# Performance work log

Measured on AMD Instinct MI355X. Metric: run time of the kernel, lower is better.

The kernel has to match this reference:

```python
import jax, jax.numpy as jnp
import numpy as np

SEQ_LEN, PRED_LEN = 512, 96
D_MODEL, D_STATE, D_FF = 512, 16, 512
DT_RANK = 32  # ceil(d_model / 16)
E_LAYERS = 2
B, N = 32, 256


def _layernorm(x, g, b, eps=1e-5):
    mu = jnp.mean(x, -1, keepdims=True)
    var = jnp.mean((x - mu) ** 2, -1, keepdims=True)
    return (x - mu) * jax.lax.rsqrt(var + eps) * g + b


def _mamba(x, win, convw, convb, wx, wdt, bdt, alog, dparam, wout):
    # x: [B, T, D] with T = n_variates + 6 (inverted tokens)
    Bb, T, D = x.shape
    xz = x @ win.T                      # [B, T, 2D] (expand=1 -> d_inner = D)
    xr, z = xz[..., :D], xz[..., D:]
    # causal depthwise conv, d_conv=2: y[t] = w0*x[t-1] + w1*x[t] + b
    x_prev = jnp.pad(xr, ((0, 0), (1, 0), (0, 0)))[:, :T]
    xc = jax.nn.silu(x_prev * convw[:, 0] + xr * convw[:, 1] + convb)
    dbl = xc @ wx.T                     # [B, T, dt_rank + 2*d_state]
    dt = jax.nn.softplus(dbl[..., :DT_RANK] @ wdt.T + bdt)     # [B, T, D]
    Bm = dbl[..., DT_RANK:DT_RANK + D_STATE]                    # [B, T, S]
    Cm = dbl[..., DT_RANK + D_STATE:]                           # [B, T, S]
    A = -jnp.exp(alog)                                          # [D, S]
    dA = jnp.exp(dt[..., None] * A)                             # [B, T, D, S]
    dBx = dt[..., None] * Bm[:, :, None, :] * xc[..., None]     # [B, T, D, S]

    def step(h, inp):
        a_t, bx_t = inp
        h = a_t * h + bx_t
        return h, h

    h0 = jnp.zeros((Bb, D, D_STATE), x.dtype)
    _, hs = jax.lax.scan(step, h0, (jnp.swapaxes(dA, 0, 1), jnp.swapaxes(dBx, 0, 1)))
    y = jnp.einsum('tbds,bts->btd', hs, Cm) + dparam * xc
    y = y * jax.nn.silu(z)
    return y @ wout.T


def _forward(x_enc, x_mark_enc, emb_w, emb_b, m_win, m_convw, m_convb, m_wx, m_wdt,
             m_bdt, m_alog, m_dparam, m_wout, ln1_g, ln1_b, ff1_w, ff1_b, ff2_w,
             ff2_b, ln2_g, ln2_b, lnf_g, lnf_b, proj_w, proj_b):
    n_var = x_enc.shape[2]
    # instance norm over time (use_norm=True)
    means = jnp.mean(x_enc, 1, keepdims=True)
    xn = x_enc - means
    stdev = jnp.sqrt(jnp.var(xn, axis=1, keepdims=True) + 1e-5)
    xn = xn / stdev
    # inverted embedding: tokens = variates (+ time-feature channels), proj seq_len -> d_model
    tok = jnp.concatenate([jnp.swapaxes(xn, 1, 2), jnp.swapaxes(x_mark_enc, 1, 2)], axis=1)
    h = tok @ emb_w.T + emb_b           # [B, n_var+6, d_model]
    for l in range(E_LAYERS):
        f = _mamba(h, m_win[l, 0], m_convw[l, 0], m_convb[l, 0], m_wx[l, 0],
                   m_wdt[l, 0], m_bdt[l, 0], m_alog[l, 0], m_dparam[l, 0], m_wout[l, 0])
        r = jnp.flip(_mamba(jnp.flip(h, 1), m_win[l, 1], m_convw[l, 1], m_convb[l, 1],
                            m_wx[l, 1], m_wdt[l, 1], m_bdt[l, 1], m_alog[l, 1],
                            m_dparam[l, 1], m_wout[l, 1]), 1)
        h = _layernorm(h + f + r, ln1_g[l], ln1_b[l])
        y = jax.nn.relu(h @ ff1_w[l].T + ff1_b[l]) @ ff2_w[l].T + ff2_b[l]
        h = _layernorm(h + y, ln2_g[l], ln2_b[l])
    h = _layernorm(h, lnf_g, lnf_b)
    dec = jnp.swapaxes(h @ proj_w.T + proj_b, 1, 2)[:, :, :n_var]  # [B, pred_len, N]
    dec = dec * stdev[:, 0, :][:, None, :] + means[:, 0, :][:, None, :]
    return dec


def setup_inputs() -> dict:
    key = jax.random.key(0)
    ks = iter(jax.random.split(key, 64))

    def rn(shape, scale=0.02):
        return jax.random.normal(next(ks), shape, dtype=jnp.float32) * scale

    D, S, R, L = D_MODEL, D_STATE, DT_RANK, E_LAYERS
    return dict(
        x_enc=jax.random.normal(next(ks), (B, SEQ_LEN, N), dtype=jnp.float32),
        x_mark_enc=jax.random.uniform(next(ks), (B, SEQ_LEN, 6), dtype=jnp.float32,
                                      minval=-1.0, maxval=1.0),
        emb_w=rn((D, SEQ_LEN)), emb_b=jnp.zeros((D,), jnp.float32),
        m_win=rn((L, 2, 2 * D, D)),
        m_convw=rn((L, 2, D, 2), 0.5),
        m_convb=jnp.zeros((L, 2, D), jnp.float32),
        m_wx=rn((L, 2, R + 2 * S, D)),
        m_wdt=rn((L, 2, D, R)),
        m_bdt=jnp.full((L, 2, D), -4.6, jnp.float32),  # softplus ~= 0.01
        m_alog=jnp.broadcast_to(jnp.log(jnp.arange(1, S + 1, dtype=jnp.float32)), (L, 2, D, S)) * jnp.ones((L, 2, D, S), jnp.float32),
        m_dparam=jnp.ones((L, 2, D), jnp.float32),
        m_wout=rn((L, 2, D, D)),
        ln1_g=jnp.ones((L, D), jnp.float32), ln1_b=jnp.zeros((L, D), jnp.float32),
        ff1_w=rn((L, D_FF, D)), ff1_b=jnp.zeros((L, D_FF), jnp.float32),
        ff2_w=rn((L, D, D_FF)), ff2_b=jnp.zeros((L, D), jnp.float32),
        ln2_g=jnp.ones((L, D), jnp.float32), ln2_b=jnp.zeros((L, D), jnp.float32),
        lnf_g=jnp.ones((D,), jnp.float32), lnf_b=jnp.zeros((D,), jnp.float32),
        proj_w=rn((PRED_LEN, D)), proj_b=jnp.zeros((PRED_LEN,), jnp.float32),
    )


def reference(x_enc, x_mark_enc, emb_w, emb_b, m_win, m_convw, m_convb, m_wx, m_wdt,
              m_bdt, m_alog, m_dparam, m_wout, ln1_g, ln1_b, ff1_w, ff1_b, ff2_w,
              ff2_b, ln2_g, ln2_b, lnf_g, lnf_b, proj_w, proj_b):
    return _forward(x_enc, x_mark_enc, emb_w, emb_b, m_win, m_convw, m_convb, m_wx,
                    m_wdt, m_bdt, m_alog, m_dparam, m_wout, ln1_g, ln1_b, ff1_w,
                    ff1_b, ff2_w, ff2_b, ln2_g, ln2_b, lnf_g, lnf_b, proj_w, proj_b)
```

## Files before the change

kernel.cpp:

```cpp
#include <hip/hip_runtime.h>
#include <hip/hip_bf16.h>
#include <math.h>
#include <stddef.h>

#define BB 32
#define TT 262
#define DD 512
#define SS 16
#define RR 32
#define SEQ 512
#define NV 256
#define PRED 96
#define MROWS (BB*TT)
#define NCHK 8
#define CSZ 33

typedef __attribute__((ext_vector_type(4))) float f32x4;
typedef __attribute__((ext_vector_type(8))) short s16x8;

__device__ inline ushort f2bu(float x) {
    __hip_bfloat16 h = __float2bfloat16(x);
    ushort u; __builtin_memcpy(&u, &h, 2); return u;
}
__device__ inline float bu2f(ushort u) {
    __hip_bfloat16 h; __builtin_memcpy(&h, &u, 2);
    return __bfloat162float(h);
}

__device__ inline void gload_lds16(const void* g, void* l) {
    __builtin_amdgcn_global_load_lds(
        (const __attribute__((address_space(1))) void*)g,
        (__attribute__((address_space(3))) void*)l, 16, 0, 0);
}

__global__ __launch_bounds__(256)
void packall(const float* __restrict__ s0, ushort* __restrict__ d0,
             const float* __restrict__ s1, ushort* __restrict__ d1,
             const float* __restrict__ s2, ushort* __restrict__ d2,
             const float* __restrict__ s3, ushort* __restrict__ d3,
             const float* __restrict__ s4, ushort* __restrict__ d4,
             const float* __restrict__ s5, ushort* __restrict__ d5)
{
    int idx = blockIdx.x * 256 + threadIdx.x;
    const float* s; ushort* dst; int o;
    if      (idx < 262144)  { s = s0; dst = d0; o = idx; }
    else if (idx < 2359296) { s = s1; dst = d1; o = idx - 262144; }
    else if (idx < 3407872) { s = s2; dst = d2; o = idx - 2359296; }
    else if (idx < 3932160) { s = s3; dst = d3; o = idx - 3407872; }
    else if (idx < 4456448) { s = s4; dst = d4; o = idx - 3932160; }
    else if (idx < 4505600) { s = s5; dst = d5; o = idx - 4456448; }
    else return;
    dst[o] = f2bu(s[o]);
}

__global__ __launch_bounds__(256)
void mkcomb(const float* __restrict__ wx, const float* __restrict__ wdt,
            ushort* __restrict__ comb)
{
    int n  = blockIdx.x;
    int li = blockIdx.y;
    const float* wxl = wx + (size_t)li*64*512;
    ushort* outb = comb + ((size_t)li*544 + n)*512;
    if (n < 512) {
        __shared__ float wr[32];
        if (threadIdx.x < 32)
            wr[threadIdx.x] = wdt[(size_t)li*512*32 + (size_t)n*32 + threadIdx.x];
        __syncthreads();
        for (int kk = threadIdx.x; kk < 512; kk += 256) {
            float acc = 0.f;
            #pragma unroll
            for (int r = 0; r < 32; ++r)
                acc = fmaf(wr[r], wxl[r*512 + kk], acc);
            outb[kk] = f2bu(acc);
        }
    } else {
        int s = n - 512;
        for (int kk = threadIdx.x; kk < 512; kk += 256)
            outb[kk] = f2bu(wxl[(32+s)*512 + kk]);
    }
}

__global__ __launch_bounds__(256)
void stats_kernel(const float* __restrict__ x_enc,
                  float* __restrict__ mean, float* __restrict__ stdv)
{
    int b  = blockIdx.x >> 4;
    int n0 = (blockIdx.x & 15) << 4;
    int nl = threadIdx.x & 15;
    int tg = threadIdx.x >> 4;
    int n = n0 + nl;
    const float* base = x_enc + (size_t)b*SEQ*NV + n;
    float s0 = 0.f, s1 = 0.f, q0 = 0.f, q1 = 0.f;
    #pragma unroll 8
    for (int i = 0; i < 16; ++i) {
        int t = tg + i*32;
        float v0 = base[(size_t)t*NV];
        float v1 = base[(size_t)(t+16)*NV];
        s0 += v0; q0 = fmaf(v0, v0, q0);
        s1 += v1; q1 = fmaf(v1, v1, q1);
    }
    float s = s0 + s1, q = q0 + q1;
    __shared__ float ls[16][17], lq[16][17];
    ls[tg][nl] = s; lq[tg][nl] = q;
    __syncthreads();
    if (tg < 8) { ls[tg][nl] += ls[tg+8][nl]; lq[tg][nl] += lq[tg+8][nl]; }
    __syncthreads();
    if (tg < 4) { ls[tg][nl] += ls[tg+4][nl]; lq[tg][nl] += lq[tg+4][nl]; }
    __syncthreads();
    if (tg < 2) { ls[tg][nl] += ls[tg+2][nl]; lq[tg][nl] += lq[tg+2][nl]; }
    __syncthreads();
    if (tg == 0) {
        s = ls[0][nl] + ls[1][nl];
        q = lq[0][nl] + lq[1][nl];
        float mu  = s * (1.f/SEQ);
        float var = q * (1.f/SEQ) - mu*mu;
        mean[b*NV + n] = mu;
        stdv[b*NV + n] = sqrtf(var + 1e-5f);
    }
}

__global__ __launch_bounds__(256)
void tok_kernel(const float* __restrict__ x_enc, const float* __restrict__ x_mark,
                const float* __restrict__ mean, const float* __restrict__ stdv,
                ushort* __restrict__ tokb)
{
    int b  = blockIdx.x / 40;
    int r  = blockIdx.x % 40;
    int tt = r / 5;
    int vt = r % 5;
    int t0 = tt << 6, v0 = vt << 6;
    __shared__ float tile[64][65];
    int lv = threadIdx.x & 63;
    for (int i = threadIdx.x >> 6; i < 64; i += 4) {
        int t = t0 + i, v = v0 + lv;
        float val = 0.f;
        if (v < NV) {
            val = (x_enc[((size_t)b*SEQ + t)*NV + v] - mean[b*NV + v]) / stdv[b*NV + v];
        } else if (v < TT) {
            val = x_mark[((size_t)b*SEQ + t)*6 + (v - NV)];
        }
        tile[i][lv] = val;
    }
    __syncthreads();
    for (int i = threadIdx.x >> 6; i < 64; i += 4) {
        int v = v0 + i;
        if (v < TT) {
            size_t row = (size_t)b*TT + v;
            tokb[row*512 + t0 + lv] = f2bu(tile[lv][i]);
        }
    }
}

template<int HAS_BIAS, int RELU, int WF32, int W3, int SCANEP>
__global__ __launch_bounds__(256)
void gemm3(const ushort* __restrict__ A3, int lda3,
           const ushort* __restrict__ W3p, int ldw3,
           const float* __restrict__ bias,
           float* __restrict__ C, int ldc,
           ushort* __restrict__ C3, int N_out,
           float* __restrict__ bcbuf,
           size_t aOff, size_t wOff, size_t biasOff, size_t cOff, size_t bcOff,
           int M, int Nn, int K3)
{
    const int dir = blockIdx.y;
    A3  += (size_t)dir * aOff;
    W3p += (size_t)dir * wOff;
    if (HAS_BIAS || SCANEP) bias += (size_t)dir * biasOff;
    if (WF32) C += (size_t)dir * cOff;
    if (W3 || SCANEP) C3 += (size_t)dir * cOff;
    if (SCANEP) bcbuf += (size_t)dir * bcOff;

    __shared__ ushort lds[2][192*64];
    const int tid  = threadIdx.x;
    const int lane = tid & 63;
    const int wid  = tid >> 6;
    const int wr = wid >> 1, wc = wid & 1;

    int nwg = gridDim.x;
    int q8 = nwg >> 3, r8 = nwg & 7;
    int xcd = blockIdx.x & 7;
    int idx = blockIdx.x >> 3;
    int swz = (xcd < r8 ? xcd*(q8+1) : r8*(q8+1) + (xcd-r8)*q8) + idx;
    int ntile = (Nn + 63) >> 6;
    const int m0 = (swz / ntile) * 128;
    const int n0 = (swz % ntile) * 64;

    const int l8 = lane >> 3;
    const int sl = lane & 7;
    const int ssl = sl ^ l8;

    int arow[4], wrow[2];
    #pragma unroll
    for (int qq = 0; qq < 4; ++qq) {
        int r = (wid*4 + qq)*8 + l8;
        int ar = m0 + r; if (ar > M-1) ar = M-1;
        arow[qq] = ar;
    }
    #pragma unroll
    for (int qq = 0; qq < 2; ++qq) {
        int r = (wid*2 + qq)*8 + l8;
        int wrr = n0 + r; if (wrr > Nn-1) wrr = Nn-1;
        wrow[qq] = wrr;
    }

    f32x4 acc[4][2];
    #pragma unroll
    for (int i = 0; i < 4; ++i)
        #pragma unroll
        for (int j = 0; j < 2; ++j) acc[i][j] = (f32x4){0.f,0.f,0.f,0.f};

    const int nk = K3 >> 6;
    const int rl = lane & 15;
    const int kq = lane >> 4;

    auto stage = [&](int buf_, int kt_) {
        #pragma unroll
        for (int qq = 0; qq < 4; ++qq) {
            int c = wid*4 + qq;
            gload_lds16(A3 + (size_t)arow[qq]*lda3 + kt_*64 + ssl*8,
                        (void*)&lds[buf_][c*512]);
        }
        #pragma unroll
        for (int qq = 0; qq < 2; ++qq) {
            int c = wid*2 + qq;
            gload_lds16(W3p + (size_t)wrow[qq]*ldw3 + kt_*64 + ssl*8,
                        (void*)&lds[buf_][8192 + c*512]);
        }
    };

    stage(0, 0);
    __syncthreads();

    for (int kt = 0; kt < nk; ++kt) {
        int cur = kt & 1;
        if (kt + 1 < nk) stage(cur ^ 1, kt + 1);
        #pragma unroll
        for (int kk = 0; kk < 2; ++kk) {
            s16x8 av[4], wv[2];
            #pragma unroll
            for (int mi = 0; mi < 4; ++mi) {
                int row = wr*64 + mi*16 + rl;
                int ck = (kk*4 + kq) ^ (row & 7);
                av[mi] = *(const s16x8*)&lds[cur][row*64 + (ck<<3)];
            }
            #pragma unroll
            for (int ni = 0; ni < 2; ++ni) {
                int row = wc*32 + ni*16 + rl;
                int ck = (kk*4 + kq) ^ (row & 7);
                wv[ni] = *(const s16x8*)&lds[cur][8192 + row*64 + (ck<<3)];
            }
            #pragma unroll
            for (int mi = 0; mi < 4; ++mi)
                #pragma unroll
                for (int ni = 0; ni < 2; ++ni)
                    acc[mi][ni] = __builtin_amdgcn_mfma_f32_16x16x32_bf16(
                        av[mi], wv[ni], acc[mi][ni], 0, 0, 0);
        }
        __syncthreads();
    }

    #pragma unroll
    for (int ni = 0; ni < 2; ++ni) {
        int n = n0 + wc*32 + ni*16 + rl;
        if (n >= Nn) continue;
        float bv = (HAS_BIAS && !SCANEP) ? bias[n] : 0.f;
        #pragma unroll
        for (int mi = 0; mi < 4; ++mi) {
            #pragma unroll
            for (int j = 0; j < 4; ++j) {
                int m = m0 + wr*64 + mi*16 + kq*4 + j;
                if (m >= M) continue;
                float v = acc[mi][ni][j];
                if (SCANEP) {
                    if (n < 512) {
                        v += bias[n];
                        v = fmaxf(v, 0.f) + log1pf(__expf(-fabsf(v)));
                        C3[(size_t)m*ldc + n] = f2bu(v);
                    } else {
                        bcbuf[(size_t)m*N_out + (n - 512)] = v;
                    }
                } else {
                    if (HAS_BIAS) v += bv;
                    if (RELU) v = fmaxf(v, 0.f);
                    if (WF32) C[(size_t)m*ldc + n] = v;
                    if (W3)   C3[(size_t)m*N_out + n] = f2bu(v);
                }
            }
        }
    }
}

__global__ __launch_bounds__(256)
void conv2(ushort* __restrict__ xzb, const float* __restrict__ cwB,
           const float* __restrict__ cbB, float* __restrict__ xc,
           ushort* __restrict__ xcb)
{
    int gid = blockIdx.x * 256 + threadIdx.x;
    int d = gid & 511;
    int r = gid >> 9;
    int dir = (r >= MROWS) ? 1 : 0;
    int bt = r - dir*MROWS;
    int t = bt % TT;
    const float* cw = cwB + dir*DD*2;
    const float* cb = cbB + dir*DD;
    size_t base = (size_t)bt*2048 + (size_t)dir*1024;
    float cur = bu2f(xzb[base + d]);
    int tn = dir ? t + 1 : t - 1;
    float prev = 0.f;
    if (tn >= 0 && tn < TT)
        prev = bu2f(xzb[base + (dir ? 2048 : -2048) + d]);
    float v = prev*cw[d*2] + cur*cw[d*2+1] + cb[d];
    float sv = v / (1.f + __expf(-v));
    size_t o = (size_t)bt*1024 + dir*512 + d;
    xc[o] = sv;
    xcb[o] = f2bu(sv);
    float z = bu2f(xzb[base + 512 + d]);
    xzb[base + 512 + d] = f2bu(z / (1.f + __expf(-z)));
}

__global__ __launch_bounds__(64)
void scan_p1(const ushort* __restrict__ sp_g, const float* __restrict__ xc_g,
             const float* __restrict__ bc_g, const float* __restrict__ alog,
             float* __restrict__ hs, float* __restrict__ ps)
{
    int dir = blockIdx.z;
    int rev = dir;
    sp_g += dir*512; xc_g += dir*512; bc_g += dir*32;
    alog += (size_t)dir*DD*SS;
    size_t doff = (size_t)dir*(NCHK-1)*65536*4;
    hs += doff; ps += doff;

    int sblk = blockIdx.x;
    int c    = blockIdx.y;
    int b  = sblk >> 3;
    int d  = ((sblk & 7) << 6) + threadIdx.x;

    float Ac[16];
    #pragma unroll
    for (int j = 0; j < 16; ++j)
        Ac[j] = -__expf(alog[d*SS + j]);

    float h[16], pp[16];
    #pragma unroll
    for (int j = 0; j < 16; ++j) { h[j] = 0.f; pp[j] = 1.f; }

    size_t bbase = (size_t)b*TT;
    int t0 = c*CSZ;
    for (int i = 0; i < CSZ; ++i) {
        int t = t0 + i;
        size_t p = bbase + (rev ? TT-1-t : t);
        float spv = bu2f(sp_g[p*1024 + d]);
        float xcv = xc_g[p*1024 + d];
        const float* bc = bc_g + p*64;
        float dtxc = spv*xcv;
        f32x4 Bq[4];
        #pragma unroll
        for (int q = 0; q < 4; ++q) Bq[q] = ((const f32x4*)bc)[q];
        #pragma unroll
        for (int j = 0; j < 16; ++j) {
            float e = __expf(spv*Ac[j]);
            h[j] = fmaf(e, h[j], dtxc*Bq[j>>2][j&3]);
            pp[j] *= e;
        }
    }
    size_t o = (((size_t)c*256 + sblk)*64 + threadIdx.x)*4;
    #pragma unroll
    for (int q = 0; q < 4; ++q) {
        ((f32x4*)hs)[o + q] = (f32x4){h[q*4+0], h[q*4+1], h[q*4+2], h[q*4+3]};
        ((f32x4*)ps)[o + q] = (f32x4){pp[q*4+0], pp[q*4+1], pp[q*4+2], pp[q*4+3]};
    }
}

__global__ __launch_bounds__(256)
void scan_comb(const float* __restrict__ hs, const float* __restrict__ ps,
               float* __restrict__ hin)
{
    int dir = blockIdx.y;
    size_t doff = (size_t)dir*(NCHK-1)*65536;
    size_t gid = (size_t)blockIdx.x*256 + threadIdx.x;
    float4 h = {0.f,0.f,0.f,0.f};
    for (int c = 0; c < NCHK-1; ++c) {
        size_t o = doff + (size_t)c*65536 + gid;
        float4 hl = ((const float4*)hs)[o];
        float4 pv = ((const float4*)ps)[o];
        h.x = fmaf(pv.x, h.x, hl.x);
        h.y = fmaf(pv.y, h.y, hl.y);
        h.z = fmaf(pv.z, h.z, hl.z);
        h.w = fmaf(pv.w, h.w, hl.w);
        ((float4*)hin)[o] = h;
    }
}

__global__ __launch_bounds__(64)
void scan_p2(const ushort* __restrict__ sp_g, const float* __restrict__ xc_g,
             const ushort* __restrict__ xz_u, const float* __restrict__ bc_g,
             const float* __restrict__ alog, const float* __restrict__ dparam,
             const float* __restrict__ hin, ushort* __restrict__ yb)
{
    int dir = blockIdx.z;
    int rev = dir;
    sp_g += dir*512; xc_g += dir*512; bc_g += dir*32; xz_u += dir*1024;
    alog += (size_t)dir*DD*SS; dparam += (size_t)dir*DD;
    hin += (size_t)dir*(NCHK-1)*65536*4;
    yb  += (size_t)dir*(size_t)MROWS*512;

    int sblk = blockIdx.x;
    int c    = blockIdx.y;
    int b  = sblk >> 3;
    int d  = ((sblk & 7) << 6) + threadIdx.x;

    float Ac[16];
    #pragma unroll
    for (int j = 0; j < 16; ++j)
        Ac[j] = -__expf(alog[d*SS + j]);
    float dp = dparam[d];

    float h[16];
    #pragma unroll
    for (int j = 0; j < 16; ++j) h[j] = 0.f;
    if (c > 0) {
        size_t o = (((size_t)(c-1)*256 + sblk)*64 + threadIdx.x)*4;
        #pragma unroll
        for (int q = 0; q < 4; ++q) {
            f32x4 hv = ((const f32x4*)hin)[o + q];
            h[q*4+0]=hv[0]; h[q*4+1]=hv[1]; h[q*4+2]=hv[2]; h[q*4+3]=hv[3];
        }
    }

    size_t bbase = (size_t)b*TT;
    int t0 = c*CSZ;
    for (int i = 0; i < CSZ; ++i) {
        int t = t0 + i;
        int tc = t < TT ? t : TT-1;
        size_t p = bbase + (rev ? TT-1-tc : tc);
        float spv = bu2f(sp_g[p*1024 + d]);
        float xcv = xc_g[p*1024 + d];
        float zsv = bu2f(xz_u[p*2048 + 512 + d]);
        const float* bc = bc_g + p*64;
        float dtxc = spv*xcv;
        f32x4 Bq[4], Cq[4];
        #pragma unroll
        for (int q = 0; q < 4; ++q) {
            Bq[q] = ((const f32x4*)bc)[q];
            Cq[q] = ((const f32x4*)(bc + 16))[q];
        }
        #pragma unroll
        for (int j = 0; j < 16; ++j) {
            float e = __expf(spv*Ac[j]);
            h[j] = fmaf(e, h[j], dtxc*Bq[j>>2][j&3]);
        }
        float p0 = 0.f, p1 = 0.f, p2 = 0.f, p3 = 0.f;
        #pragma unroll
        for (int q = 0; q < 4; ++q) {
            p0 = fmaf(h[q*4+0], Cq[q][0], p0);
            p1 = fmaf(h[q*4+1], Cq[q][1], p1);
            p2 = fmaf(h[q*4+2], Cq[q][2], p2);
            p3 = fmaf(h[q*4+3], Cq[q][3], p3);
        }
        float dot = (p0 + p1) + (p2 + p3);
        if (t < TT) {
            int tg = rev ? TT-1-t : t;
            float yv = (dot + dp*xcv) * zsv;
            yb[(bbase + tg)*512 + d] = f2bu(yv);
        }
    }
}

__global__ __launch_bounds__(64)
void ln_kernel(float* __restrict__ dst, const float* __restrict__ a,
               const float* __restrict__ b, const float* __restrict__ c,
               const float* __restrict__ g, const float* __restrict__ beta,
               ushort* __restrict__ outb)
{
    int row = blockIdx.x;
    int lane = threadIdx.x;
    size_t base = (size_t)row * DD;
    float x[8];
    #pragma unroll
    for (int j = 0; j < 2; ++j) {
        int e4 = j*64 + lane;
        float4 v = *(const float4*)(a + base + (size_t)e4*4);
        if (b) { float4 t = *(const float4*)(b + base + (size_t)e4*4); v.x+=t.x; v.y+=t.y; v.z+=t.z; v.w+=t.w; }
        if (c) { float4 t = *(const float4*)(c + base + (size_t)e4*4); v.x+=t.x; v.y+=t.y; v.z+=t.z; v.w+=t.w; }
        x[j*4+0]=v.x; x[j*4+1]=v.y; x[j*4+2]=v.z; x[j*4+3]=v.w;
    }
    float s = 0.f;
    #pragma unroll
    for (int i = 0; i < 8; ++i) s += x[i];
    #pragma unroll
    for (int m = 1; m < 64; m <<= 1) s += __shfl_xor(s, m);
    float mu = s * (1.f/DD);
    float vs = 0.f;
    #pragma unroll
    for (int i = 0; i < 8; ++i) { float dd = x[i]-mu; vs += dd*dd; }
    #pragma unroll
    for (int m = 1; m < 64; m <<= 1) vs += __shfl_xor(vs, m);
    float r = rsqrtf(vs*(1.f/DD) + 1e-5f);
    #pragma unroll
    for (int j = 0; j < 2; ++j) {
        int e4 = j*64 + lane;
        float4 gv = *(const float4*)(g    + (size_t)e4*4);
        float4 bv = *(const float4*)(beta + (size_t)e4*4);
        float4 o;
        o.x = (x[j*4+0]-mu)*r*gv.x + bv.x;
        o.y = (x[j*4+1]-mu)*r*gv.y + bv.y;
        o.z = (x[j*4+2]-mu)*r*gv.z + bv.z;
        o.w = (x[j*4+3]-mu)*r*gv.w + bv.w;
        *(float4*)(dst + base + (size_t)e4*4) = o;
        if (outb) {
            ushort* ob = outb + (size_t)row*512;
            ob[e4*4+0] = f2bu(o.x);
            ob[e4*4+1] = f2bu(o.y);
            ob[e4*4+2] = f2bu(o.z);
            ob[e4*4+3] = f2bu(o.w);
        }
    }
}

__global__ __launch_bounds__(256)
void proj_fin(const float* __restrict__ projtmp, const float* __restrict__ mean,
              const float* __restrict__ stdv, float* __restrict__ out)
{
    int b  = blockIdx.x >> 2;
    int n0 = (blockIdx.x & 3) << 6;
    __shared__ float tile[64][97];
    for (int i = threadIdx.x; i < 64*96; i += 256) {
        int rj = i / 96, cp = i % 96;
        tile[rj][cp] = projtmp[((size_t)b*TT + n0 + rj)*96 + cp];
    }
    __syncthreads();
    int nl = threadIdx.x & 63;
    int pg = threadIdx.x >> 6;
    int n = n0 + nl;
    float sd = stdv[b*NV + n];
    float mu = mean[b*NV + n];
    #pragma unroll
    for (int i = 0; i < 24; ++i) {
        int p = pg*24 + i;
        out[((size_t)b*PRED + p)*NV + n] = tile[nl][p]*sd + mu;
    }
}

extern "C" void kernel_launch(void* const* d_in, const int* in_sizes, int n_in,
                              void* d_out, int out_size, void* d_ws, size_t ws_size,
                              hipStream_t stream)
{
    (void)in_sizes; (void)n_in; (void)out_size; (void)ws_size;
    const float* x_enc   = (const float*)d_in[0];
    const float* x_mark  = (const float*)d_in[1];
    const float* emb_w   = (const float*)d_in[2];
    const float* emb_b   = (const float*)d_in[3];
    const float* m_win   = (const float*)d_in[4];
    const float* m_convw = (const float*)d_in[5];
    const float* m_convb = (const float*)d_in[6];
    const float* m_wx    = (const float*)d_in[7];
    const float* m_wdt   = (const float*)d_in[8];
    const float* m_bdt   = (const float*)d_in[9];
    const float* m_alog  = (const float*)d_in[10];
    const float* m_dpar  = (const float*)d_in[11];
    const float* m_wout  = (const float*)d_in[12];
    const float* ln1_g   = (const float*)d_in[13];
    const float* ln1_b   = (const float*)d_in[14];
    const float* ff1_w   = (const float*)d_in[15];
    const float* ff1_b   = (const float*)d_in[16];
    const float* ff2_w   = (const float*)d_in[17];
    const float* ff2_b   = (const float*)d_in[18];
    const float* ln2_g   = (const float*)d_in[19];
    const float* ln2_b   = (const float*)d_in[20];
    const float* lnf_g   = (const float*)d_in[21];
    const float* lnf_b   = (const float*)d_in[22];
    const float* proj_w  = (const float*)d_in[23];
    const float* proj_b  = (const float*)d_in[24];
    float* out = (float*)d_out;

    float* ws = (float*)d_ws;
    const size_t NBT = (size_t)MROWS;
    size_t off = 0;
    float* mean = ws + off; off += 8192;
    float* stdv = ws + off; off += 8192;
    ushort* w_emb  = (ushort*)(ws + off); off += 131072;
    ushort* w_win  = (ushort*)(ws + off); off += 1048576;
    ushort* w_wout = (ushort*)(ws + off); off += 524288;
    ushort* w_ff1  = (ushort*)(ws + off); off += 262144;
    ushort* w_ff2  = (ushort*)(ws + off); off += 262144;
    ushort* w_comb = (ushort*)(ws + off); off += 557056;
    ushort* w_proj = (ushort*)(ws + off); off += 24576;
    ushort* pool = (ushort*)(ws + off); off += NBT*768;
    ushort* tokb = pool;
    ushort* xcb  = pool;
    ushort* yb   = pool;
    float* h   = ws + off; off += NBT*512;
    ushort* hb = (ushort*)(ws + off); off += NBT*256;
    ushort* xzb = (ushort*)(ws + off); off += NBT*1024;
    ushort* fftb = xzb;
    ushort* spb = (ushort*)(ws + off); off += NBT*512;
    float* xc  = ws + off; off += NBT*1024;
    float* bc2 = ws + off; off += NBT*64;
    float* fbuf = ws + off; off += NBT*512;
    float* rbuf = ws + off; off += NBT*512;
    float* hs  = ws + off; off += (size_t)2*(NCHK-1)*65536*4;
    float* psb = ws + off; off += (size_t)2*(NCHK-1)*65536*4;
    float* hin = ws + off; off += (size_t)2*(NCHK-1)*65536*4;
    float* projtmp = ws + off; off += NBT*96;
    (void)rbuf;

    packall<<<dim3((4505600+255)/256), 256, 0, stream>>>(
        emb_w, w_emb, m_win, w_win, m_wout, w_wout,
        ff1_w, w_ff1, ff2_w, w_ff2, proj_w, w_proj);
    mkcomb<<<dim3(544,4), 256, 0, stream>>>(m_wx, m_wdt, w_comb);

    stats_kernel<<<dim3(BB*16), 256, 0, stream>>>(x_enc, mean, stdv);
    tok_kernel<<<dim3(BB*40), 256, 0, stream>>>(x_enc, x_mark, mean, stdv, tokb);

    gemm3<1,0,1,1,0><<<dim3(66*8), 256, 0, stream>>>(tokb, 512, w_emb, 512,
        emb_b, h, DD, hb, 512, nullptr, 0,0,0,0,0, MROWS, 512, 512);

    for (int l = 0; l < 2; ++l) {
        gemm3<0,0,0,1,0><<<dim3(66*32), 256, 0, stream>>>(hb, 512,
            w_win + (size_t)l*2048*512, 512, nullptr,
            nullptr, 0, xzb, 2048, nullptr, 0,0,0,0,0, MROWS, 2048, 512);
        conv2<<<dim3((2*MROWS*DD)/256), 256, 0, stream>>>(xzb,
            m_convw + (size_t)l*2*DD*2, m_convb + (size_t)l*2*DD, xc, xcb);
        gemm3<0,0,0,0,1><<<dim3(66*9, 2), 256, 0, stream>>>(
            xcb, 1024, w_comb + (size_t)l*2*544*512, 512,
            m_bdt + (size_t)l*2*DD, nullptr, 1024, spb, 64, bc2,
            512, (size_t)544*512, 512,
            512, 32, MROWS, 544, 512);
        const float* al = m_alog + (size_t)l*2*DD*SS;
        const float* dpp = m_dpar + (size_t)l*2*DD;
        scan_p1<<<dim3(256, NCHK-1, 2), 64, 0, stream>>>(spb, xc, bc2, al,
            hs, psb);
        scan_comb<<<dim3(256, 2), 256, 0, stream>>>(hs, psb, hin);
        scan_p2<<<dim3(256, NCHK, 2), 64, 0, stream>>>(spb, xc, xzb, bc2,
            al, dpp, hin, yb);
        gemm3<0,0,1,0,0><<<dim3(66*8, 2), 256, 0, stream>>>(yb, 512,
            w_wout + (size_t)l*2*512*512, 512, nullptr,
            fbuf, DD, nullptr, 0, nullptr,
            NBT*512, (size_t)512*512, 0,
            NBT*512, 0, MROWS, 512, 512);
        ln_kernel<<<dim3(MROWS), 64, 0, stream>>>(h, h, fbuf, rbuf,
            ln1_g + l*DD, ln1_b + l*DD, hb);
        gemm3<1,1,0,1,0><<<dim3(66*8), 256, 0, stream>>>(hb, 512,
            w_ff1 + (size_t)l*512*512, 512, ff1_b + l*DD,
            nullptr, 0, fftb, 512, nullptr, 0,0,0,0,0, MROWS, 512, 512);
        gemm3<1,0,1,0,0><<<dim3(66*8), 256, 0, stream>>>(fftb, 512,
            w_ff2 + (size_t)l*512*512, 512, ff2_b + l*DD,
            xc, DD, nullptr, 0, nullptr, 0,0,0,0,0, MROWS, 512, 512);
        ln_kernel<<<dim3(MROWS), 64, 0, stream>>>(h, h, xc, nullptr,
            ln2_g + l*DD, ln2_b + l*DD, hb);
    }
    ln_kernel<<<dim3(MROWS), 64, 0, stream>>>(fbuf, h, nullptr, nullptr,
                                              lnf_g, lnf_b, hb);
    gemm3<1,0,1,0,0><<<dim3(66*2), 256, 0, stream>>>(hb, 512, w_proj, 512,
        proj_b, projtmp, 96, nullptr, 0, nullptr, 0,0,0,0,0, MROWS, 96, 512);
    proj_fin<<<dim3(BB*4), 256, 0, stream>>>(projtmp, mean, stdv, out);
}
```

Before: 623.9 us.

## Fuse bidirectional out-projections into one K=1024 GEMM and use fast softplus

The forward and reverse Mamba outputs are now written side by side into a single [M,1024] buffer. The out-projection weights are repacked into a [512,1024] layout, so one GEMM with K=1024 produces the sum of both directions directly. This drops the batched two-GEMM launch, the separate fp32 rbuf output and the extra add in layernorm. The softplus epilogue also swaps log1pf for the fast __logf(1+x), which may cost a little accuracy for small values.

```diff
diff --git a/kernel.cpp b/kernel.cpp
--- a/kernel.cpp
+++ b/kernel.cpp
@@ -42,14 +42,23 @@
              const float* __restrict__ s5, ushort* __restrict__ d5)
 {
     int idx = blockIdx.x * 256 + threadIdx.x;
+    if (idx >= 4505600) return;
+    if (idx >= 2359296 && idx < 3407872) {
+        int o = idx - 2359296;
+        int l   = o >> 19;
+        int rem = o & 524287;
+        int dir = rem >> 18;
+        int n   = (rem >> 9) & 511;
+        int k   = rem & 511;
+        d2[((size_t)(l*512 + n))*1024 + dir*512 + k] = f2bu(s2[o]);
+        return;
+    }
     const float* s; ushort* dst; int o;
     if      (idx < 262144)  { s = s0; dst = d0; o = idx; }
     else if (idx < 2359296) { s = s1; dst = d1; o = idx - 262144; }
-    else if (idx < 3407872) { s = s2; dst = d2; o = idx - 2359296; }
     else if (idx < 3932160) { s = s3; dst = d3; o = idx - 3407872; }
     else if (idx < 4456448) { s = s4; dst = d4; o = idx - 3932160; }
-    else if (idx < 4505600) { s = s5; dst = d5; o = idx - 4456448; }
-    else return;
+    else                    { s = s5; dst = d5; o = idx - 4456448; }
     dst[o] = f2bu(s[o]);
 }
 
@@ -274,7 +283,7 @@
                 if (SCANEP) {
                     if (n < 512) {
                         v += bias[n];
-                        v = fmaxf(v, 0.f) + log1pf(__expf(-fabsf(v)));
+                        v = fmaxf(v, 0.f) + __logf(1.f + __expf(-fabsf(v)));
                         C3[(size_t)m*ldc + n] = f2bu(v);
                     } else {
                         bcbuf[(size_t)m*N_out + (n - 512)] = v;
@@ -402,7 +411,7 @@
     sp_g += dir*512; xc_g += dir*512; bc_g += dir*32; xz_u += dir*1024;
     alog += (size_t)dir*DD*SS; dparam += (size_t)dir*DD;
     hin += (size_t)dir*(NCHK-1)*65536*4;
-    yb  += (size_t)dir*(size_t)MROWS*512;
+    yb  += dir*512;
 
     int sblk = blockIdx.x;
     int c    = blockIdx.y;
@@ -461,7 +470,7 @@
         if (t < TT) {
             int tg = rev ? TT-1-t : t;
             float yv = (dot + dp*xcv) * zsv;
-            yb[(bbase + tg)*512 + d] = f2bu(yv);
+            yb[(bbase + tg)*1024 + d] = f2bu(yv);
         }
     }
 }
@@ -597,12 +606,10 @@
     float* xc  = ws + off; off += NBT*1024;
     float* bc2 = ws + off; off += NBT*64;
     float* fbuf = ws + off; off += NBT*512;
-    float* rbuf = ws + off; off += NBT*512;
     float* hs  = ws + off; off += (size_t)2*(NCHK-1)*65536*4;
     float* psb = ws + off; off += (size_t)2*(NCHK-1)*65536*4;
     float* hin = ws + off; off += (size_t)2*(NCHK-1)*65536*4;
     float* projtmp = ws + off; off += NBT*96;
-    (void)rbuf;
 
     packall<<<dim3((4505600+255)/256), 256, 0, stream>>>(
         emb_w, w_emb, m_win, w_win, m_wout, w_wout,
@@ -633,12 +640,11 @@
         scan_comb<<<dim3(256, 2), 256, 0, stream>>>(hs, psb, hin);
         scan_p2<<<dim3(256, NCHK, 2), 64, 0, stream>>>(spb, xc, xzb, bc2,
             al, dpp, hin, yb);
-        gemm3<0,0,1,0,0><<<dim3(66*8, 2), 256, 0, stream>>>(yb, 512,
-            w_wout + (size_t)l*2*512*512, 512, nullptr,
+        gemm3<0,0,1,0,0><<<dim3(66*8), 256, 0, stream>>>(yb, 1024,
+            w_wout + (size_t)l*512*1024, 1024, nullptr,
             fbuf, DD, nullptr, 0, nullptr,
-            NBT*512, (size_t)512*512, 0,
-            NBT*512, 0, MROWS, 512, 512);
-        ln_kernel<<<dim3(MROWS), 64, 0, stream>>>(h, h, fbuf, rbuf,
+            0,0,0,0,0, MROWS, 512, 1024);
+        ln_kernel<<<dim3(MROWS), 64, 0, stream>>>(h, h, fbuf, nullptr,
             ln1_g + l*DD, ln1_b + l*DD, hb);
         gemm3<1,1,0,1,0><<<dim3(66*8), 256, 0, stream>>>(hb, 512,
             w_ff1 + (size_t)l*512*512, 512, ff1_b + l*DD,
```

Result: faster. 564.6 us (-9.5%).
